# Optimization experiments

Hardware: AMD Instinct MI355X
Metric: run time of the kernel (lower is better)

## Reference

```python
import jax, jax.numpy as jnp
import numpy as np
import math

B, LL, LP, H, C, S, T = 16, 512, 2048, 1024, 8192, 10, 4
PAD_TOKEN_ID = 2000
VAR_TOKEN_BASE = 2001


def _attend(q, k, v):
    # q: [b,q,h], k/v: [b,k,h]
    scores = jnp.einsum('bqh,bkh->bqk', q, k) / math.sqrt(float(q.shape[-1]))
    w = jax.nn.softmax(scores, axis=-1)
    return jnp.einsum('bqk,bkh->bqh', w, v)


def _gru_cell(x, h, Wih, Whh, bih, bhh):
    gi = x @ Wih + bih   # [B,3H], gate order r,z,n (torch GRUCell)
    gh = h @ Whh + bhh
    i_r, i_z, i_n = jnp.split(gi, 3, axis=-1)
    h_r, h_z, h_n = jnp.split(gh, 3, axis=-1)
    r = jax.nn.sigmoid(i_r + h_r)
    z = jax.nn.sigmoid(i_z + h_z)
    n = jnp.tanh(i_n + r * h_n)
    return (1.0 - z) * n + z * h


def setup_inputs() -> dict:
    key = jax.random.key(0)
    ks = jax.random.split(key, 18)
    def lin(k, i, o):
        return jax.random.normal(k, (i, o), jnp.float32) * 0.02
    return {
        'logic_hidden': jax.random.normal(ks[0], (B, LL, H), jnp.float32),
        'prompt_hidden': jax.random.normal(ks[1], (B, LP, H), jnp.float32),
        'codebook_emb': jax.random.normal(ks[2], (C, H), jnp.float32) * 0.02,
        'W_init': lin(ks[3], 2 * H, H),
        'W_pq': lin(ks[4], H, H),
        'W_pk': lin(ks[5], H, H),
        'W_pv': lin(ks[6], H, H),
        'slot_queries': jax.random.normal(ks[7], (S - 1, H), jnp.float32) * 0.02,
        'W_sq': lin(ks[8], H, H),
        'W_op': lin(ks[9], H, H),
        'W_gate': lin(ks[10], H, 1),
        'b_gate': jnp.zeros((1,), jnp.float32),
        'W_stop': lin(ks[11], 2 * H, 1),
        'b_stop': jnp.zeros((1,), jnp.float32),
        'gru_Wih': lin(ks[12], H, 3 * H),
        'gru_Whh': lin(ks[13], H, 3 * H),
        'gru_bih': jnp.zeros((3 * H,), jnp.float32),
        'gru_bhh': jnp.zeros((3 * H,), jnp.float32),
    }


def reference(logic_hidden, prompt_hidden, codebook_emb, W_init, W_pq, W_pk, W_pv,
              slot_queries, W_sq, W_op, W_gate, b_gate, W_stop, b_stop,
              gru_Wih, gru_Whh, gru_bih, gru_bhh):
    batch = logic_hidden.shape[0]
    prompt_summary = prompt_hidden.mean(axis=1)
    logic_summary = logic_hidden.mean(axis=1)
    state = jnp.tanh(jnp.concatenate([prompt_summary, logic_summary], axis=-1) @ W_init)
    pk = prompt_hidden @ W_pk   # [B,LP,H]
    pv = prompt_hidden @ W_pv
    cb_sq = jnp.sum(codebook_emb * codebook_emb, axis=-1)   # [C]
    slot_idx = jnp.arange(S - 1, dtype=jnp.int64)[None, :].repeat(batch, axis=0)

    summaries, stop_logits, stop_probs = [], [], []
    for _ in range(T):
        state_q = (state @ W_pq)[:, None, :]
        state_ctx = _attend(state_q, pk, pv)[:, 0, :]         # [B,H]
        op_pre = state_ctx @ W_op
        # squared euclidean distance to codebook without [B,C,H] diff tensor
        dist = (jnp.sum(op_pre * op_pre, axis=-1, keepdims=True)
                - 2.0 * (op_pre @ codebook_emb.T) + cb_sq[None, :])  # [B,C]
        op_logits = -dist
        op_idx = jnp.argmax(op_logits, axis=-1)               # [B]
        op_embedding = codebook_emb[op_idx]                   # [B,H]
        slot_seed = state_ctx[:, None, :] + slot_queries[None, :, :]   # [B,S-1,H]
        slot_q = slot_seed @ W_sq
        slot_tensors = _attend(slot_q, pk, pv)                # [B,S-1,H]
        slot_use_probs = jax.nn.sigmoid((slot_seed @ W_gate)[..., 0] + b_gate[0])  # [B,S-1]
        slot_mask = slot_use_probs >= 0.5
        # fallback if no slot selected anywhere in the batch (global check, as in torch)
        fb_mask = jax.nn.one_hot(jnp.argmax(slot_use_probs, axis=-1), S - 1, dtype=jnp.bool_)
        slot_mask = jnp.where(jnp.any(slot_mask), slot_mask, fb_mask)
        mf = slot_mask.astype(slot_tensors.dtype)
        slot_summary = jnp.sum(slot_tensors * mf[..., None], axis=1) / \
            jnp.clip(jnp.sum(mf, axis=-1, keepdims=True), 1.0)
        matrix_summary = jnp.tanh(op_embedding + slot_summary)
        stop_logit = (jnp.concatenate([state_ctx, matrix_summary], axis=-1) @ W_stop)[:, 0] + b_stop[0]
        summaries.append(matrix_summary)
        stop_logits.append(stop_logit)
        stop_probs.append(jax.nn.sigmoid(stop_logit))
        state = _gru_cell(matrix_summary, state, gru_Wih, gru_Whh, gru_bih, gru_bhh)

    stop_logits_t = jnp.stack(stop_logits, axis=1)   # [B,T]
    stop_probs_t = jnp.stack(stop_probs, axis=1)
    summary_stack = jnp.stack(summaries, axis=1)     # [B,T,H]
    stop_hits = stop_probs_t >= 0.5
    chain_lengths = jnp.argmax(stop_hits.astype(jnp.int64), axis=1) + 1
    chain_lengths = jnp.where(jnp.sum(stop_hits, axis=1) == 0,
                              jnp.full_like(chain_lengths, T), chain_lengths)
    return summary_stack, stop_logits_t, stop_probs_t, chain_lengths
```

## Files before the change

### kernel.cpp

```cpp
#include <hip/hip_runtime.h>


#define DINL __device__ __forceinline__

DINL float dot4(float4 a, float4 b) {
  return fmaf(a.x, b.x, fmaf(a.y, b.y, fmaf(a.z, b.z, a.w * b.w)));
}
DINL unsigned sortable(float f) {
  unsigned u = __float_as_uint(f);
  return (u & 0x80000000u) ? ~u : (u | 0x80000000u);
}
#define AXPY4(A, W, P) \
  { A.x = fmaf(W, P.x, A.x); A.y = fmaf(W, P.y, A.y); A.z = fmaf(W, P.z, A.z); A.w = fmaf(W, P.w, A.w); }
#define ADD4(A, V) { A.x += V.x; A.y += V.y; A.z += V.z; A.w += V.w; }

static constexpr int F_CBSQ  = 0;
static constexpr int F_STATE = F_CBSQ + 8192;
static constexpr int F_WQK   = F_STATE + 16384;
static constexpr int F_T1    = F_WQK + 1048576;
static constexpr int F_WFUSE = F_T1 + 1048576;
static constexpr int F_SQKCP = F_WFUSE + 2105344;
static constexpr int F_E     = F_SQKCP + 36928;
static constexpr int F_PMP   = F_E + 294912;
static constexpr int F_LMP   = F_PMP + 1048576;
static constexpr int F_MEAN  = F_LMP + 262144;
static constexpr int F_S2P   = F_MEAN + 32768;
static constexpr int F_WQKP  = F_S2P + 131072;
static constexpr int F_T1P   = F_WQKP + 4194304;
static constexpr int F_WFP   = F_T1P + 4194304;
static constexpr int F_QS1   = F_WFP + 8421376;
static constexpr int F_ACCSM = F_QS1 + 131072;
static constexpr int F_LSM   = F_ACCSM + 1048576;
static constexpr int F_CTX   = F_LSM + 1024;
static constexpr int F_FWP   = F_CTX + 16384;
static constexpr int F_OPV   = F_FWP + 526336;
static constexpr int F_OPMAX = F_OPV + 16384;
static constexpr int F_OPIDX = F_OPMAX + 16384;
static constexpr int F_GPRE  = F_OPIDX + 64;
static constexpr int F_GC    = F_GPRE + 64;
static constexpr int F_STOPA = F_GC + 64;
static constexpr int F_QSLB  = F_STOPA + 64;
static constexpr int F_LPS   = F_QSLB + 16384;
static constexpr int F_SSUM  = F_LPS + 4672;
static constexpr int F_MS    = F_SSUM + 16384;
static constexpr int F_GP    = F_MS + 16384;
static constexpr int F_K8P   = F_GP + 786432;
static constexpr int F_ACCP  = F_K8P + 262144;

struct SG {
  const float* Bm;
  const float* Bg;
  const float* a0;
  float* out;
  int M, N, Ncore, NB, kslice, ksh, lda, ldb, ldo, mr;
  float scale;
};

template <int MR>
DINL void sgemm_body(const SG p, int bx, float* As) {
  const int t = threadIdx.x;
  const int ks = bx / p.NB, nb = bx % p.NB;
  const int kslice = p.kslice;
  const int kb = ks * kslice;
  const int tot = p.M * kslice;
  for (int idx = t; idx < tot; idx += 256) {
    const int m = idx >> p.ksh;
    const int kl = idx & (kslice - 1);
    As[(m << p.ksh) + kl] = p.a0[m * p.lda + kb + kl];
  }
  __syncthreads();
  const int nl = t & 63, mg = t >> 6;
  const int n = nb * 64 + nl;
  const bool nok = (n < p.N);
  float acc[MR];
#pragma unroll
  for (int i = 0; i < MR; i++) acc[i] = 0.f;
  const bool useg = nok && (n >= p.Ncore);
  const float* Bc = p.Bm + n;
  for (int k4 = 0; k4 < kslice; k4 += 4) {
    float bv[4];
#pragma unroll
    for (int u = 0; u < 4; u++) {
      bv[u] = 0.f;
      if (nok) bv[u] = useg ? p.Bg[kb + k4 + u] : Bc[(kb + k4 + u) * p.ldb];
    }
#pragma unroll
    for (int i = 0; i < MR; i++) {
      const int m = mg + 4 * i;
      if (MR == 4 || m < p.M) {
        const float4 av = *(const float4*)&As[(m << p.ksh) + k4];
        acc[i] = fmaf(av.x, bv[0], acc[i]);
        acc[i] = fmaf(av.y, bv[1], acc[i]);
        acc[i] = fmaf(av.z, bv[2], acc[i]);
        acc[i] = fmaf(av.w, bv[3], acc[i]);
      }
    }
  }
  if (nok) {
#pragma unroll
    for (int i = 0; i < MR; i++) {
      const int m = mg + 4 * i;
      if (MR == 4 || m < p.M) p.out[(ks * p.M + m) * p.ldo + n] = acc[i] * p.scale;
    }
  }
}

DINL int sw4(int c) { return c ^ (((c >> 5) & 3) << 2); }

DINL void ph_wgT(int bx, float* sm, const float* __restrict__ A1,
                 const float* __restrict__ B, float* __restrict__ C1P,
                 const float* __restrict__ A2, float* __restrict__ C2P) {
  float* As = sm;
  float* Bs = sm + 2112;
  const int which = bx >> 8;
  const int rem = bx & 255;
  const int ks = rem >> 6;
  const int tile = rem & 63;
  const int bi = tile >> 3, bj = tile & 7;
  const float* A = which ? A2 : A1;
  float* CP = (which ? C2P : C1P) + ks * 1048576;
  const int t = threadIdx.x;
  const int sr = t >> 2, q4 = t & 3;
  const int tr = (t >> 4) << 3, tc = (t & 15) << 3;
  const int stc0 = sw4(tc), stc1 = sw4(tc + 4);
  float acc[8][8];
#pragma unroll
  for (int i = 0; i < 8; i++)
#pragma unroll
    for (int j = 0; j < 8; j++) acc[i][j] = 0.f;

  const int k00 = ks * 256;
  for (int k0 = k00; k0 < k00 + 256; k0 += 16) {
    __syncthreads();
#pragma unroll
    for (int h = 0; h < 2; h++) {
      const int r = sr + h * 64;
      const float4 av = *(const float4*)&A[(bi * 128 + r) * 1024 + k0 + q4 * 4];
      const float4 bv = *(const float4*)&B[(bj * 128 + r) * 1024 + k0 + q4 * 4];
      As[(q4 * 4 + 0) * 132 + r] = av.x; As[(q4 * 4 + 1) * 132 + r] = av.y;
      As[(q4 * 4 + 2) * 132 + r] = av.z; As[(q4 * 4 + 3) * 132 + r] = av.w;
      const int swr = sw4(r);
      Bs[(q4 * 4 + 0) * 132 + swr] = bv.x; Bs[(q4 * 4 + 1) * 132 + swr] = bv.y;
      Bs[(q4 * 4 + 2) * 132 + swr] = bv.z; Bs[(q4 * 4 + 3) * 132 + swr] = bv.w;
    }
    __syncthreads();
#pragma unroll
    for (int kk = 0; kk < 16; kk++) {
      const float* ar = &As[kk * 132];
      const float* br = &Bs[kk * 132];
      const float4 a0 = *(const float4*)&ar[tr];
      const float4 a1 = *(const float4*)&ar[tr + 4];
      const float4 b0 = *(const float4*)&br[stc0];
      const float4 b1 = *(const float4*)&br[stc1];
      const float a[8] = {a0.x, a0.y, a0.z, a0.w, a1.x, a1.y, a1.z, a1.w};
      const float b[8] = {b0.x, b0.y, b0.z, b0.w, b1.x, b1.y, b1.z, b1.w};
#pragma unroll
      for (int i = 0; i < 8; i++)
#pragma unroll
        for (int j = 0; j < 8; j++) acc[i][j] = fmaf(a[i], b[j], acc[i][j]);
    }
  }
#pragma unroll
  for (int i = 0; i < 8; i++) {
    const int row = bi * 128 + tr + i;
    *(float4*)&CP[row * 1024 + bj * 128 + tc] =
        make_float4(acc[i][0], acc[i][1], acc[i][2], acc[i][3]);
    *(float4*)&CP[row * 1024 + bj * 128 + tc + 4] =
        make_float4(acc[i][4], acc[i][5], acc[i][6], acc[i][7]);
  }
}

DINL void ph_wgF(int bx, float* sm, const float* __restrict__ Wpv,
                 const float* __restrict__ Wop, const float* __restrict__ T1,
                 float* __restrict__ CfP) {
  float* As = sm;
  float* Bs = sm + 2112;
  const int ks = bx >> 7;
  const int rem = bx & 127;
  const int bi = rem >> 4, bj = rem & 15;
  const float* Bsrc = (bj < 8) ? (Wop + bj * 128) : (T1 + (bj - 8) * 128);
  float* CP = CfP + ks * 2105344;
  const int t = threadIdx.x;
  const int sr = t >> 2, q4 = t & 3;
  const int kkq = t >> 4, c8 = (t & 15) << 3;
  const int tr = (t >> 4) << 3, tc = (t & 15) << 3;
  const int stc0 = sw4(tc), stc1 = sw4(tc + 4);
  float acc[8][8];
#pragma unroll
  for (int i = 0; i < 8; i++)
#pragma unroll
    for (int j = 0; j < 8; j++) acc[i][j] = 0.f;

  const int k00 = ks * 256;
  for (int k0 = k00; k0 < k00 + 256; k0 += 16) {
    __syncthreads();
#pragma unroll
    for (int h = 0; h < 2; h++) {
      const int r = sr + h * 64;
      const float4 av = *(const float4*)&Wpv[(bi * 128 + r) * 1024 + k0 + q4 * 4];
      As[(q4 * 4 + 0) * 132 + r] = av.x; As[(q4 * 4 + 1) * 132 + r] = av.y;
      As[(q4 * 4 + 2) * 132 + r] = av.z; As[(q4 * 4 + 3) * 132 + r] = av.w;
    }
    {
      const float4 v0 = *(const float4*)&Bsrc[(k0 + kkq) * 1024 + c8];
      const float4 v1 = *(const float4*)&Bsrc[(k0 + kkq) * 1024 + c8 + 4];
      *(float4*)&Bs[kkq * 132 + sw4(c8)] = v0;
      *(float4*)&Bs[kkq * 132 + sw4(c8 + 4)] = v1;
    }
    __syncthreads();
#pragma unroll
    for (int kk = 0; kk < 16; kk++) {
      const float* ar = &As[kk * 132];
      const float* br = &Bs[kk * 132];
      const float4 a0 = *(const float4*)&ar[tr];
      const float4 a1 = *(const float4*)&ar[tr + 4];
      const float4 b0 = *(const float4*)&br[stc0];
      const float4 b1 = *(const float4*)&br[stc1];
      const float a[8] = {a0.x, a0.y, a0.z, a0.w, a1.x, a1.y, a1.z, a1.w};
      const float b[8] = {b0.x, b0.y, b0.z, b0.w, b1.x, b1.y, b1.z, b1.w};
#pragma unroll
      for (int i = 0; i < 8; i++)
#pragma unroll
        for (int j = 0; j < 8; j++) acc[i][j] = fmaf(a[i], b[j], acc[i][j]);
    }
  }
#pragma unroll
  for (int i = 0; i < 8; i++) {
    const int row = bi * 128 + tr + i;
    *(float4*)&CP[row * 2056 + bj * 128 + tc] =
        make_float4(acc[i][0], acc[i][1], acc[i][2], acc[i][3]);
    *(float4*)&CP[row * 2056 + bj * 128 + tc + 4] =
        make_float4(acc[i][4], acc[i][5], acc[i][6], acc[i][7]);
  }
}

DINL void ph_meanpsum(int vb, const float* __restrict__ src,
                      float* __restrict__ out, int R) {
  const int s = vb >> 4, b = vb & 15, t = threadIdx.x;
  const float4* base = (const float4*)src + (size_t)(b * R + s * 32) * 256 + t;
  float4 acc = make_float4(0.f, 0.f, 0.f, 0.f);
#pragma unroll 4
  for (int r = 0; r < 32; r++) {
    const float4 v = base[r * 256];
    ADD4(acc, v);
  }
  ((float4*)out)[((s * 16 + b) << 8) + t] = acc;
}

DINL void ph_cbsq(int vb, const float* __restrict__ cbv, float* __restrict__ out) {
  const int c = vb * 4 + (threadIdx.x >> 6);
  const int l = threadIdx.x & 63;
  const float4* cr = (const float4*)(cbv + (c << 10));
  float s = 0.f;
#pragma unroll
  for (int r = 0; r < 4; r++) {
    const float4 v = cr[4 * l + r];
    s += dot4(v, v);
  }
#pragma unroll
  for (int off = 32; off > 0; off >>= 1) s += __shfl_xor(s, off);
  if (l == 0) out[c] = s;
}

DINL void ph_gs(int vb, const float* __restrict__ Wpv, const float* __restrict__ Wgate,
                const float* __restrict__ Wstop, float* __restrict__ Cf) {
  const int t = threadIdx.x;
  const int row = vb * 16 + (t >> 4);
  const int lane = t & 15;
  const float* base = Wpv + row * 1024 + lane * 64;
  const float* gb = Wgate + lane * 64;
  const float* sb = Wstop + lane * 64;
  float g = 0.f, s = 0.f;
#pragma unroll 4
  for (int k = 0; k < 64; k += 4) {
    const float4 av = *(const float4*)&base[k];
    const float4 gv = *(const float4*)&gb[k];
    const float4 sv = *(const float4*)&sb[k];
    g += dot4(av, gv);
    s += dot4(av, sv);
  }
#pragma unroll
  for (int off = 8; off > 0; off >>= 1) {
    g += __shfl_xor(g, off);
    s += __shfl_xor(s, off);
  }
  if (lane == 0) {
    Cf[row * 2056 + 2048] = g;
    Cf[row * 2056 + 2049] = s;
  }
}

DINL void ph_meancat(int vb, const float* __restrict__ pmp,
                     const float* __restrict__ lmp, float* __restrict__ mean) {
  const int gi = vb * 256 + threadIdx.x;
  const int b = gi >> 11, k = gi & 2047;
  float v = 0.f;
  if (k < 1024) {
    for (int s = 0; s < 64; s++) v += pmp[((s * 16 + b) << 10) + k];
    v *= (1.f / 2048.f);
  } else {
    const int kk = k - 1024;
    for (int s = 0; s < 16; s++) v += lmp[((s * 16 + b) << 10) + kk];
    v *= (1.f / 512.f);
  }
  mean[b * 2048 + k] = v;
}

DINL void ph_combT(int vb, const float* __restrict__ C1P, const float* __restrict__ C2P,
                   float* __restrict__ C1, float* __restrict__ C2, float scale) {
  const int half = vb >> 12;
  const int i = ((vb & 4095) << 8) + threadIdx.x;
  const float* src = half ? C2P : C1P;
  float s = 0.f;
#pragma unroll
  for (int ks = 0; ks < 4; ks++) s += src[ks * 1048576 + i];
  (half ? C2 : C1)[i] = s * scale;
}

DINL void ph_combF(int vb, const float* __restrict__ CfP, float* __restrict__ Cf) {
  const int i2 = vb * 256 + threadIdx.x;
  const int r = i2 >> 11, c = i2 & 2047;
  float s = 0.f;
#pragma unroll
  for (int ks = 0; ks < 4; ks++) s += CfP[ks * 2105344 + r * 2056 + c];
  Cf[r * 2056 + c] = s;
}

DINL void ph_s2b(int vb, const float* __restrict__ s2p, float* __restrict__ state) {
  const int gi = vb * 256 + threadIdx.x;
  const int b = gi >> 10, h = gi & 1023;
  float s = 0.f;
  for (int si = 0; si < 8; si++) s += s2p[((si * 16 + b) << 10) + h];
  state[gi] = tanhf(s);
}

DINL void ph_E(int vb, char* qsm, const float* __restrict__ prompt,
               const float* __restrict__ sqkcP, float* __restrict__ E) {
  const int kc = vb & 63, b = vb >> 6;
  const int t = threadIdx.x;
  for (int idx = t; idx < 9216; idx += 256) {
    const int j = idx >> 10, h = idx & 1023;
    float s = 0.f;
    for (int sp = 0; sp < 4; sp++) s += sqkcP[(sp * 9 + j) * 1025 + h];
    const int x = idx << 2;
    *(float*)(qsm + (x ^ (((x >> 7) & 7) << 4))) = s;
  }
  __syncthreads();
  const int w = t >> 6, l = t & 63;
  const int bxl = 64 * l;
  const int key = ((bxl >> 7) & 7) << 4;
  const int o0 = bxl ^ key, o1 = (bxl + 16) ^ key, o2 = (bxl + 32) ^ key, o3 = (bxl + 48) ^ key;
  const int k0 = kc * 32 + w * 8;
  const float* pbase = prompt + ((b * 2048 + k0) << 10) + 16 * l;
  for (int ki = 0; ki < 8; ki++) {
    const float4* pr = (const float4*)(pbase + (ki << 10));
    const float4 p0 = pr[0], p1 = pr[1], p2 = pr[2], p3 = pr[3];
    float sj[9];
#pragma unroll
    for (int j = 0; j < 9; j++) {
      const char* qp = qsm + (j << 12);
      sj[j] = dot4(*(const float4*)(qp + o0), p0) + dot4(*(const float4*)(qp + o1), p1) +
              dot4(*(const float4*)(qp + o2), p2) + dot4(*(const float4*)(qp + o3), p3);
    }
#pragma unroll
    for (int off = 32; off > 0; off >>= 1) {
#pragma unroll
      for (int j = 0; j < 9; j++) sj[j] += __shfl_xor(sj[j], off);
    }
    float wv = sj[0];
#pragma unroll
    for (int j = 1; j < 9; j++)
      if (l == j) wv = sj[j];
    if (l < 9) E[(b * 2048 + k0 + ki) * 9 + l] = __expf(wv);
  }
}

__global__ __launch_bounds__(256) void k_setup1(const float* prompt, const float* logic,
                                                const float* cbv, const float* Wpv,
                                                const float* Wgate, const float* Wstop,
                                                const float* Wpq, const float* Wsq,
                                                const float* Wpk, float* w) {
  __shared__ __align__(16) float sm[4224];
  const int bx = blockIdx.x;
  if (bx < 512) ph_wgT(bx, sm, Wpq, Wpk, w + F_WQKP, Wsq, w + F_T1P);
  else if (bx < 1536) ph_meanpsum(bx - 512, prompt, w + F_PMP, 2048);
  else if (bx < 1792) ph_meanpsum(bx - 1536, logic, w + F_LMP, 512);
  else if (bx < 3840) ph_cbsq(bx - 1792, cbv, w + F_CBSQ);
  else ph_gs(bx - 3840, Wpv, Wgate, Wstop, w + F_WFUSE);
}

__global__ __launch_bounds__(256) void k_setup2(float* w, float scale) {
  const int bx = blockIdx.x;
  if (bx < 8192) ph_combT(bx, w + F_WQKP, w + F_T1P, w + F_WQK, w + F_T1, scale);
  else ph_meancat(bx - 8192, w + F_PMP, w + F_LMP, w + F_MEAN);
}

__global__ __launch_bounds__(256) void k_setup3(SG pInit, SG pSqkc,
                                                const float* Wpv, const float* Wop,
                                                float* w) {
  __shared__ __align__(16) float As[4352];
  const int bx = blockIdx.x;
  if (bx < 512) ph_wgF(bx, As, Wpv, Wop, w + F_T1, w + F_WFP);
  else if (bx < 640) sgemm_body<4>(pInit, bx - 512, As);
  else sgemm_body<7>(pSqkc, bx - 640, As);
}

__global__ __launch_bounds__(256) void k_setup4(const float* prompt, float* w) {
  __shared__ __align__(16) char qsm[36864];
  const int bx = blockIdx.x;
  if (bx < 1024) ph_E(bx, qsm, prompt, w + F_SQKCP, w + F_E);
  else if (bx < 9216) ph_combF(bx - 1024, w + F_WFP, w + F_WFUSE);
  else ph_s2b(bx - 9216, w + F_S2P, w + F_STATE);
}


DINL void ph_qs1(int bx, char* smemc, const float* state, const float* Wqk,
                 float* outP) {
  float* As = (float*)smemc;
  const int t = threadIdx.x;
  const int ks = bx >> 4, nb = bx & 15;
  const int kb = ks * 128;
  for (int idx = t; idx < 2048; idx += 256)
    As[idx] = state[((idx >> 7) << 10) + kb + (idx & 127)];
  __syncthreads();
  const int nl = t & 63, mg = t >> 6;
  const int n = nb * 64 + nl;
  const float* Bc = Wqk + n;
  float acc[4] = {0.f, 0.f, 0.f, 0.f};
  for (int k4 = 0; k4 < 128; k4 += 4) {
    float bv[4];
#pragma unroll
    for (int u = 0; u < 4; u++) bv[u] = Bc[(kb + k4 + u) << 10];
#pragma unroll
    for (int i = 0; i < 4; i++) {
      const float4 av = *(const float4*)&As[((mg + 4 * i) << 7) + k4];
      acc[i] = fmaf(av.x, bv[0], acc[i]);
      acc[i] = fmaf(av.y, bv[1], acc[i]);
      acc[i] = fmaf(av.z, bv[2], acc[i]);
      acc[i] = fmaf(av.w, bv[3], acc[i]);
    }
  }
#pragma unroll
  for (int i = 0; i < 4; i++)
    outP[((ks * 16 + mg + 4 * i) << 10) + n] = acc[i];
}

DINL void ph_flash(int g, int b, char* smemc, const float* prompt,
                   const float* qs1P, float* accsm, float* lsm) {
  float* red = (float*)smemc;
  float* lred = (float*)(smemc + 16384);
  const int t = threadIdx.x;
  const int w = t >> 6, l = t & 63;
  float4 q0 = make_float4(0.f, 0.f, 0.f, 0.f), q1 = q0, q2 = q0, q3 = q0;
#pragma unroll
  for (int s = 0; s < 8; s++) {
    const float4* qp = (const float4*)(qs1P + ((s * 16 + b) << 10) + 16 * l);
    ADD4(q0, qp[0]); ADD4(q1, qp[1]); ADD4(q2, qp[2]); ADD4(q3, qp[3]);
  }
  float4 acc[4];
#pragma unroll
  for (int r = 0; r < 4; r++) acc[r] = make_float4(0.f, 0.f, 0.f, 0.f);
  float lsum = 0.f;
  const int k0 = g * 32 + w * 8;
  const float* pbase = prompt + ((b * 2048 + k0) << 10) + 16 * l;
#pragma unroll 2
  for (int k = 0; k < 8; k++) {
    const float4* pr = (const float4*)(pbase + (k << 10));
    const float4 p0 = pr[0], p1 = pr[1], p2 = pr[2], p3 = pr[3];
    float s = dot4(q0, p0) + dot4(q1, p1) + dot4(q2, p2) + dot4(q3, p3);
#pragma unroll
    for (int off = 32; off > 0; off >>= 1) s += __shfl_xor(s, off);
    const float wgt = __expf(s);
    lsum += wgt;
    AXPY4(acc[0], wgt, p0); AXPY4(acc[1], wgt, p1);
    AXPY4(acc[2], wgt, p2); AXPY4(acc[3], wgt, p3);
  }
  float4* myr = (float4*)(red + w * 1024 + 16 * l);
  myr[0] = acc[0]; myr[1] = acc[1]; myr[2] = acc[2]; myr[3] = acc[3];
  if (l == 0) lred[w] = lsum;
  __syncthreads();
  float4 s0 = *(float4*)(red + t * 4);
  const float4 s1 = *(float4*)(red + 1024 + t * 4);
  const float4 s2 = *(float4*)(red + 2048 + t * 4);
  const float4 s3 = *(float4*)(red + 3072 + t * 4);
  ADD4(s0, s1); ADD4(s0, s2); ADD4(s0, s3);
  *(float4*)&accsm[((b * 64 + g) << 10) + t * 4] = s0;
  if (t == 0) lsm[b * 64 + g] = lred[0] + lred[1] + lred[2] + lred[3];
}

DINL void ph_cst(int bx, char* smemc, const float* accsm, const float* lsm,
                 float* ctx) {
  float4* sred = (float4*)smemc;
  float* rinvp = (float*)(smemc + 4096);
  const int b = bx >> 4, hq = bx & 15;
  const int t = threadIdx.x;
  if (t < 64) {
    float s = lsm[b * 64 + t];
#pragma unroll
    for (int off = 32; off > 0; off >>= 1) s += __shfl_xor(s, off);
    if (t == 0) rinvp[0] = 1.f / s;
  }
  const int h4 = hq * 16 + (t & 15);
  const int gp = t >> 4;
  float4 a = make_float4(0.f, 0.f, 0.f, 0.f);
#pragma unroll
  for (int gi = 0; gi < 4; gi++) {
    const int g = gp * 4 + gi;
    const float4 v = ((const float4*)accsm)[((b * 64 + g) << 8) + h4];
    ADD4(a, v);
  }
  sred[t] = a;
  __syncthreads();
  if (t < 16) {
    float4 s = sred[t];
    for (int p2 = 1; p2 < 16; p2++) {
      const float4 v = sred[p2 * 16 + t];
      ADD4(s, v);
    }
    const float rinv = rinvp[0];
    s.x *= rinv; s.y *= rinv; s.z *= rinv; s.w *= rinv;
    ((float4*)ctx)[(b << 8) + hq * 16 + t] = s;
  }
}

DINL void ph_fw(int bx, char* smemc, const float* ctx, const float* wfuse,
                float* outp) {
  float* As = (float*)smemc;
  const int t = threadIdx.x;
  const int ks = bx / 33, nb = bx % 33;
  const int kb = ks * 64;
  for (int idx = t; idx < 1024; idx += 256)
    As[idx] = ctx[((idx >> 6) << 10) + kb + (idx & 63)];
  __syncthreads();
  const int nl = t & 63, mg = t >> 6;
  const int n = nb * 64 + nl;
  const bool nok = (n < 2050);
  const float* Bc = wfuse + n;
  float acc[4] = {0.f, 0.f, 0.f, 0.f};
  for (int k4 = 0; k4 < 64; k4 += 4) {
    float bv[4];
#pragma unroll
    for (int u = 0; u < 4; u++) bv[u] = nok ? Bc[(kb + k4 + u) * 2056] : 0.f;
#pragma unroll
    for (int i = 0; i < 4; i++) {
      const float4 av = *(const float4*)&As[((mg + 4 * i) << 6) + k4];
      acc[i] = fmaf(av.x, bv[0], acc[i]);
      acc[i] = fmaf(av.y, bv[1], acc[i]);
      acc[i] = fmaf(av.z, bv[2], acc[i]);
      acc[i] = fmaf(av.w, bv[3], acc[i]);
    }
  }
  if (nok) {
#pragma unroll
    for (int i = 0; i < 4; i++) outp[(ks * 16 + mg + 4 * i) * 2056 + n] = acc[i];
  }
}

DINL void ph_combw(int bx, const float* fwP, const float* sqkcP, float* opv,
                   float* qslb, float* gpre, float* gc, float* stopA) {
  const int t = threadIdx.x;
  if (bx < 64) {
    const int i = bx * 256 + t;
    const int b = i >> 10, h = i & 1023;
    float s = 0.f;
    for (int p = 0; p < 16; p++) s += fwP[(p * 16 + b) * 2056 + h];
    opv[i] = s;
  } else if (bx < 128) {
    const int i = (bx - 64) * 256 + t;
    const int b = i >> 10, h = i & 1023;
    float s = 0.f;
    for (int p = 0; p < 16; p++) s += fwP[(p * 16 + b) * 2056 + 1024 + h];
    qslb[i] = s;
  } else {
    if (t < 16) {
      float g = 0.f, sa = 0.f;
      for (int p = 0; p < 16; p++) {
        g += fwP[(p * 16 + t) * 2056 + 2048];
        sa += fwP[(p * 16 + t) * 2056 + 2049];
      }
      gpre[t] = g;
      stopA[t] = sa;
    } else if (t < 25) {
      const int j = t - 16;
      float g = 0.f;
      for (int sp = 0; sp < 4; sp++) g += sqkcP[(sp * 9 + j) * 1025 + 1024];
      gc[j] = g;
    }
  }
}

DINL void ph_slot(int vb, char* smemc, const float* prompt, const float* qslb,
                  const float* E, float* accp, float* lpsum) {
  float* wl = (float*)smemc;
  float* lred = (float*)(smemc + 2560);
  const int kc = vb & 31, b = vb >> 5;
  const int t = threadIdx.x;
  const int w = t >> 6, l = t & 63;
  const float4* qp = (const float4*)(qslb + (b << 10) + 16 * l);
  const float4 q0 = qp[0], q1 = qp[1], q2 = qp[2], q3 = qp[3];
  const int kbase = kc * 64 + w * 16;
  float lacc = 0.f;
  const float* pbase = prompt + ((b * 2048 + kbase) << 10) + 16 * l;
  for (int ki = 0; ki < 16; ki++) {
    const float4* pr = (const float4*)(pbase + (ki << 10));
    const float4 p0 = pr[0], p1 = pr[1], p2 = pr[2], p3 = pr[3];
    float s = dot4(q0, p0) + dot4(q1, p1) + dot4(q2, p2) + dot4(q3, p3);
#pragma unroll
    for (int off = 32; off > 0; off >>= 1) s += __shfl_xor(s, off);
    const float we = __expf(s);
    if (l < 9) {
      const float wv = we * E[(b * 2048 + kbase + ki) * 9 + l];
      wl[(w * 16 + ki) * 10 + l] = wv;
      lacc += wv;
    }
  }
  if (l < 9) lred[w * 9 + l] = lacc;
  __syncthreads();
  if (t < 9)
    lpsum[(b * 32 + kc) * 9 + t] = lred[t] + lred[9 + t] + lred[18 + t] + lred[27 + t];
  const int h4 = (w << 8) + (l << 2);
  float4 acc[9];
#pragma unroll
  for (int j = 0; j < 9; j++) acc[j] = make_float4(0.f, 0.f, 0.f, 0.f);
  const float* pb2 = prompt + ((b * 2048 + kc * 64) << 10) + h4;
#pragma unroll 2
  for (int k = 0; k < 64; k++) {
    const float4 pv = *(const float4*)(pb2 + (k << 10));
    const float* wr = &wl[k * 10];
#pragma unroll
    for (int j = 0; j < 9; j++) AXPY4(acc[j], wr[j], pv);
  }
  float* ob = accp + (((kc * 16 + b) * 9) << 10) + h4;
#pragma unroll
  for (int j = 0; j < 9; j++) *(float4*)(ob + (j << 10)) = acc[j];
}

DINL void ph_cb(int vb, char* smemc, const float* opv, const float* cbv,
                const float* cbsqv, unsigned long long* opmaxp) {
  const int t = threadIdx.x;
  const int w = t >> 6, l = t & 63;
  const int bxl = 64 * l;
  const int key = ((bxl >> 7) & 7) << 4;
  const int o0 = bxl ^ key, o1 = (bxl + 16) ^ key, o2 = (bxl + 32) ^ key, o3 = (bxl + 48) ^ key;
  for (int half = 0; half < 2; half++) {
    __syncthreads();
    for (int idx = t; idx < 8192; idx += 256) {
      const int x = idx << 2;
      *(float*)(smemc + (x ^ (((x >> 7) & 7) << 4))) = opv[half * 8192 + idx];
    }
    __syncthreads();
    unsigned long long bk[8];
#pragma unroll
    for (int m = 0; m < 8; m++) bk[m] = 0ull;
    const int cbase = (vb << 4) + (w << 2);
    for (int ci = 0; ci < 4; ci++) {
      const int c = cbase + ci;
      const float4* cr = (const float4*)(cbv + (c << 10));
      const float4 c0 = cr[4 * l], c1 = cr[4 * l + 1], c2 = cr[4 * l + 2], c3 = cr[4 * l + 3];
      float sm[8];
#pragma unroll
      for (int m = 0; m < 8; m++) {
        const char* qp = smemc + (m << 12);
        const float4 a0 = *(const float4*)(qp + o0);
        const float4 a1 = *(const float4*)(qp + o1);
        const float4 a2 = *(const float4*)(qp + o2);
        const float4 a3 = *(const float4*)(qp + o3);
        sm[m] = dot4(a0, c0) + dot4(a1, c1) + dot4(a2, c2) + dot4(a3, c3);
      }
#pragma unroll
      for (int off = 32; off > 0; off >>= 1) {
#pragma unroll
        for (int m = 0; m < 8; m++) sm[m] += __shfl_xor(sm[m], off);
      }
      const float cq = cbsqv[c];
#pragma unroll
      for (int m = 0; m < 8; m++) {
        const float sc = fmaf(2.f, sm[m], -cq);
        const unsigned long long k2 =
            ((unsigned long long)sortable(sc) << 32) | (unsigned)(8192 - c);
        bk[m] = k2 > bk[m] ? k2 : bk[m];
      }
    }
    unsigned long long* red = (unsigned long long*)(smemc + 32768);
    __syncthreads();
    if (l == 0) {
#pragma unroll
      for (int m = 0; m < 8; m++) red[w * 8 + m] = bk[m];
    }
    __syncthreads();
    if (t < 8) {
      unsigned long long b2 = red[t];
      for (int ww = 1; ww < 4; ww++) {
        const unsigned long long v = red[ww * 8 + t];
        b2 = v > b2 ? v : b2;
      }
      opmaxp[vb * 16 + half * 8 + t] = b2;
    }
  }
}

DINL void ph_k7(int bx, char* smemc, const float* accp, const float* lpsum,
                const float* gpre_g, const float* gc_g, const float* bgate,
                const unsigned long long* opmax, int* opidx, float* ssum) {
  unsigned long long* red = (unsigned long long*)smemc;
  float* rl = (float*)(smemc + 2048);
  float* gpre = (float*)(smemc + 2112);
  float* gcs = (float*)(smemc + 2192);
  int* mask_s = (int*)(smemc + 2240);
  float* cntInvp = (float*)(smemc + 2288);
  const int t = threadIdx.x;
  if (bx == 64) {
    const int b = t & 15, part = t >> 4;
    unsigned long long best = 0ull;
    for (int c = part * 32; c < part * 32 + 32; c++) {
      const unsigned long long v = opmax[c * 16 + b];
      best = v > best ? v : best;
    }
    red[t] = best;
    __syncthreads();
    if (t < 16) {
      unsigned long long m = red[t];
      for (int p2 = 1; p2 < 16; p2++) {
        const unsigned long long v = red[p2 * 16 + t];
        m = v > m ? v : m;
      }
      opidx[t] = 8192 - (int)(unsigned)(m & 0xFFFFFFFFull);
    }
    return;
  }
  const int b = bx >> 2;
  if (t < 9) {
    float s = 0.f;
    for (int c = 0; c < 32; c++) s += lpsum[(b * 32 + c) * 9 + t];
    rl[t] = 1.f / s;
  }
  if (t >= 32 && t < 48) gpre[t - 32] = gpre_g[t - 32];
  if (t >= 48 && t < 57) gcs[t - 48] = gc_g[t - 48];
  __syncthreads();
  if (t == 0) {
    const float bg = bgate[0];
    bool any = false;
    for (int bb = 0; bb < 16; bb++)
      for (int j = 0; j < 9; j++)
        if (gpre[bb] + gcs[j] + bg >= 0.f) any = true;
    int cnt = 0;
    if (any) {
      for (int j = 0; j < 9; j++) {
        const int s = (gpre[b] + gcs[j] + bg >= 0.f) ? 1 : 0;
        mask_s[j] = s;
        cnt += s;
      }
    } else {
      float bv = -3.4e38f;
      int bj = 0;
      for (int j = 0; j < 9; j++) {
        const float v = gpre[b] + gcs[j] + bg;
        if (v > bv) { bv = v; bj = j; }
      }
      for (int j = 0; j < 9; j++) mask_s[j] = (j == bj) ? 1 : 0;
      cnt = 1;
    }
    cntInvp[0] = 1.f / (float)(cnt > 0 ? cnt : 1);
  }
  __syncthreads();
  const int h = ((bx & 3) << 8) + t;
  float v = 0.f;
  for (int j = 0; j < 9; j++) {
    if (mask_s[j]) {
      float s = 0.f;
      for (int c = 0; c < 32; c++) s += accp[(((c * 16 + b) * 9 + j) << 10) + h];
      v = fmaf(s, rl[j], v);
    }
  }
  ssum[(b << 10) + h] = v * cntInvp[0];
}

DINL void ph_k8p(int bx, char* smemc, const float* ssum, const float* Wpv,
                 float* outP) {
  float* As = (float*)smemc;
  const int t = threadIdx.x;
  const int ks = bx >> 4, nb = bx & 15;
  const int kb = ks * 64;
  for (int idx = t; idx < 1024; idx += 256)
    As[idx] = ssum[((idx >> 6) << 10) + kb + (idx & 63)];
  __syncthreads();
  const int nl = t & 63, mg = t >> 6;
  const int n = nb * 64 + nl;
  const float* Bc = Wpv + n;
  float acc[4] = {0.f, 0.f, 0.f, 0.f};
  for (int k4 = 0; k4 < 64; k4 += 4) {
    float bv[4];
#pragma unroll
    for (int u = 0; u < 4; u++) bv[u] = Bc[(kb + k4 + u) << 10];
#pragma unroll
    for (int i = 0; i < 4; i++) {
      const float4 av = *(const float4*)&As[((mg + 4 * i) << 6) + k4];
      acc[i] = fmaf(av.x, bv[0], acc[i]);
      acc[i] = fmaf(av.y, bv[1], acc[i]);
      acc[i] = fmaf(av.z, bv[2], acc[i]);
      acc[i] = fmaf(av.w, bv[3], acc[i]);
    }
  }
#pragma unroll
  for (int i = 0; i < 4; i++)
    outP[((ks * 16 + mg + 4 * i) << 10) + n] = acc[i];
}

DINL void ph_gru(int bx, char* smemc, const float* k8p, const int* opidx,
                 const float* cbv, const float* state, const float* Wih,
                 const float* Whh, float* gpP, float* ms, float* dout, int it) {
  float* As = (float*)smemc;
  const int t = threadIdx.x;
  const int half = (bx >= 384) ? 1 : 0;
  const int b2 = half ? bx - 384 : bx;
  const int ks = b2 / 48, nb = b2 % 48;
  const int kb = ks * 128;
  for (int idx = t; idx < 2048; idx += 256) {
    const int m = idx >> 7, kl = idx & 127;
    float v;
    if (!half) {
      float s = 0.f;
      for (int p = 0; p < 16; p++) s += k8p[((p * 16 + m) << 10) + kb + kl];
      v = tanhf(s + cbv[(opidx[m] << 10) + kb + kl]);
      if (nb == 0) {
        ms[(m << 10) + kb + kl] = v;
        dout[(m << 12) + (it << 10) + kb + kl] = v;
      }
    } else {
      v = state[(m << 10) + kb + kl];
    }
    As[idx] = v;
  }
  __syncthreads();
  const int nl = t & 63, mg = t >> 6;
  const int n = nb * 64 + nl;
  const float* Bc = (half ? Whh : Wih) + n;
  float acc[4] = {0.f, 0.f, 0.f, 0.f};
  for (int k4 = 0; k4 < 128; k4 += 4) {
    float bv[4];
#pragma unroll
    for (int u = 0; u < 4; u++) bv[u] = Bc[(kb + k4 + u) * 3072];
#pragma unroll
    for (int i = 0; i < 4; i++) {
      const float4 av = *(const float4*)&As[((mg + 4 * i) << 7) + k4];
      acc[i] = fmaf(av.x, bv[0], acc[i]);
      acc[i] = fmaf(av.y, bv[1], acc[i]);
      acc[i] = fmaf(av.z, bv[2], acc[i]);
      acc[i] = fmaf(av.w, bv[3], acc[i]);
    }
  }
  float* outp = gpP + half * 3072;
#pragma unroll
  for (int i = 0; i < 4; i++) outp[(ks * 16 + mg + 4 * i) * 6144 + n] = acc[i];
}

DINL void ph_k9b(int bx, const float* gp, const float* bih, const float* bhh,
                 float* state, const float* stopA, const float* ms,
                 const float* Wstop, const float* bstop, float* dout, int it) {
  const int t = threadIdx.x;
  if (bx < 64) {
    const int gi = bx * 256 + t;
    const int b = gi >> 10, h = gi & 1023;
    float ir = 0.f, iz = 0.f, inn = 0.f, hr = 0.f, hz = 0.f, hn = 0.f;
    for (int s = 0; s < 8; s++) {
      const float* g = gp + (s * 16 + b) * 6144;
      ir += g[h]; iz += g[1024 + h]; inn += g[2048 + h];
      hr += g[3072 + h]; hz += g[4096 + h]; hn += g[5120 + h];
    }
    ir += bih[h]; iz += bih[1024 + h]; inn += bih[2048 + h];
    hr += bhh[h]; hz += bhh[1024 + h]; hn += bhh[2048 + h];
    const float r = 1.f / (1.f + __expf(-(ir + hr)));
    const float z = 1.f / (1.f + __expf(-(iz + hz)));
    const float n = tanhf(fmaf(r, hn, inn));
    const float hold = state[gi];
    state[gi] = (1.f - z) * n + z * hold;
  } else {
    const int wid = (bx - 64) * 4 + (t >> 6);
    const int l = t & 63;
    float p = 0.f;
    for (int i = 0; i < 16; i++) {
      const int h = l + (i << 6);
      p = fmaf(ms[(wid << 10) + h], Wstop[1024 + h], p);
    }
#pragma unroll
    for (int off = 32; off > 0; off >>= 1) p += __shfl_xor(p, off);
    if (l == 0) {
      const float lg = p + stopA[wid] + bstop[0];
      dout[65536 + wid * 4 + it] = lg;
      dout[65600 + wid * 4 + it] = 1.f / (1.f + __expf(-lg));
    }
  }
}

__global__ __launch_bounds__(256) void kf_qs1(const float* state, const float* Wqk, float* outP) {
  __shared__ __align__(16) char smem[8192];
  ph_qs1(blockIdx.x, smem, state, Wqk, outP);
}
__global__ __launch_bounds__(256) void kf_flash(const float* prompt, const float* qs1P,
                                                float* accsm, float* lsm) {
  __shared__ __align__(16) char smem[16416];
  ph_flash(blockIdx.x, blockIdx.y, smem, prompt, qs1P, accsm, lsm);
}
__global__ __launch_bounds__(256) void kf_cst(const float* accsm, const float* lsm, float* ctx) {
  __shared__ __align__(16) char smem[4112];
  ph_cst(blockIdx.x, smem, accsm, lsm, ctx);
}
__global__ __launch_bounds__(256) void kf_fw(const float* ctx, const float* wfuse, float* outp) {
  __shared__ __align__(16) char smem[4096];
  ph_fw(blockIdx.x, smem, ctx, wfuse, outp);
}
__global__ __launch_bounds__(256) void kf_combw(const float* fwP, const float* sqkcP,
                                                float* opv, float* qslb, float* gpre,
                                                float* gc, float* stopA) {
  ph_combw(blockIdx.x, fwP, sqkcP, opv, qslb, gpre, gc, stopA);
}
__global__ __launch_bounds__(256) void k_slotcb(const float* prompt, const float* qslb,
                                                const float* E, float* accp, float* lpsum,
                                                const float* opv, const float* cbv,
                                                const float* cbsqv,
                                                unsigned long long* opmaxp) {
  __shared__ __align__(16) char smem[33024];
  const int bx = blockIdx.x;
  if (bx < 512) ph_slot(bx, smem, prompt, qslb, E, accp, lpsum);
  else ph_cb(bx - 512, smem, opv, cbv, cbsqv, opmaxp);
}
__global__ __launch_bounds__(256) void kf_k7(const float* accp, const float* lpsum,
                                             const float* gpre_g, const float* gc_g,
                                             const float* bgate,
                                             const unsigned long long* opmax,
                                             int* opidx, float* ssum) {
  __shared__ __align__(16) char smem[2304];
  ph_k7(blockIdx.x, smem, accp, lpsum, gpre_g, gc_g, bgate, opmax, opidx, ssum);
}
__global__ __launch_bounds__(256) void kf_k8p(const float* ssum, const float* Wpv, float* outP) {
  __shared__ __align__(16) char smem[4096];
  ph_k8p(blockIdx.x, smem, ssum, Wpv, outP);
}
__global__ __launch_bounds__(256) void kf_gru(const float* k8p, const int* opidx,
                                              const float* cbv, const float* state,
                                              const float* Wih, const float* Whh,
                                              float* gpP, float* ms, float* dout, int it) {
  __shared__ __align__(16) char smem[8192];
  ph_gru(blockIdx.x, smem, k8p, opidx, cbv, state, Wih, Whh, gpP, ms, dout, it);
}
__global__ __launch_bounds__(256) void kf_k9b(const float* gp, const float* bih,
                                              const float* bhh, float* state,
                                              const float* stopA, const float* ms,
                                              const float* Wstop, const float* bstop,
                                              float* dout, int it) {
  ph_k9b(blockIdx.x, gp, bih, bhh, state, stopA, ms, Wstop, bstop, dout, it);
}
__global__ void kf_k10(float* __restrict__ dout) {
  const int t = threadIdx.x;
  if (t < 16) {
    int cl = 4;
    for (int it = 0; it < 4; it++) {
      if (dout[65536 + t * 4 + it] >= 0.f) { cl = it + 1; break; }
    }
    dout[65664 + t] = (float)cl;
  }
}

extern "C" void kernel_launch(void* const* d_in, const int* in_sizes, int n_in,
                              void* d_out, int out_size, void* d_ws, size_t ws_size,
                              hipStream_t stream) {
  (void)in_sizes; (void)n_in; (void)out_size; (void)ws_size;
  const float* logic  = (const float*)d_in[0];
  const float* prompt = (const float*)d_in[1];
  const float* cbv    = (const float*)d_in[2];
  const float* W_init = (const float*)d_in[3];
  const float* W_pq   = (const float*)d_in[4];
  const float* W_pk   = (const float*)d_in[5];
  const float* W_pv   = (const float*)d_in[6];
  const float* slotq  = (const float*)d_in[7];
  const float* W_sq   = (const float*)d_in[8];
  const float* W_op   = (const float*)d_in[9];
  const float* W_gate = (const float*)d_in[10];
  const float* b_gate = (const float*)d_in[11];
  const float* W_stop = (const float*)d_in[12];
  const float* b_stop = (const float*)d_in[13];
  const float* Wih    = (const float*)d_in[14];
  const float* Whh    = (const float*)d_in[15];
  const float* bih    = (const float*)d_in[16];
  const float* bhh    = (const float*)d_in[17];
  float* out = (float*)d_out;
  float* w = (float*)d_ws;

  const float inv32 = 1.0f / 32.0f;

  k_setup1<<<3904, 256, 0, stream>>>(prompt, logic, cbv, W_pv, W_gate, W_stop,
                                     W_pq, W_sq, W_pk, w);
  k_setup2<<<8320, 256, 0, stream>>>(w, inv32);
  {
    SG pInit;
    pInit.Bm = W_init; pInit.Bg = nullptr; pInit.a0 = w + F_MEAN;
    pInit.out = w + F_S2P;
    pInit.M = 16; pInit.N = 1024; pInit.Ncore = 1024; pInit.NB = 16;
    pInit.kslice = 256; pInit.ksh = 8; pInit.lda = 2048; pInit.ldb = 1024;
    pInit.ldo = 1024; pInit.mr = 4; pInit.scale = 1.f;
    SG pSqkc;
    pSqkc.Bm = w + F_T1; pSqkc.Bg = W_gate; pSqkc.a0 = slotq;
    pSqkc.out = w + F_SQKCP;
    pSqkc.M = 9; pSqkc.N = 1025; pSqkc.Ncore = 1024; pSqkc.NB = 17;
    pSqkc.kslice = 256; pSqkc.ksh = 8; pSqkc.lda = 1024; pSqkc.ldb = 1024;
    pSqkc.ldo = 1025; pSqkc.mr = 7; pSqkc.scale = 1.f;
    k_setup3<<<708, 256, 0, stream>>>(pInit, pSqkc, W_pv, W_op, w);
  }
  k_setup4<<<9280, 256, 0, stream>>>(prompt, w);

  for (int it = 0; it < 4; ++it) {
    kf_qs1<<<128, 256, 0, stream>>>(w + F_STATE, w + F_WQK, w + F_QS1);
    kf_flash<<<dim3(64, 16), 256, 0, stream>>>(prompt, w + F_QS1,
                                               w + F_ACCSM, w + F_LSM);
    kf_cst<<<256, 256, 0, stream>>>(w + F_ACCSM, w + F_LSM, w + F_CTX);
    kf_fw<<<528, 256, 0, stream>>>(w + F_CTX, w + F_WFUSE, w + F_FWP);
    kf_combw<<<129, 256, 0, stream>>>(w + F_FWP, w + F_SQKCP, w + F_OPV,
                                      w + F_QSLB, w + F_GPRE, w + F_GC, w + F_STOPA);
    k_slotcb<<<1024, 256, 0, stream>>>(prompt, w + F_QSLB, w + F_E,
                                       w + F_ACCP, w + F_LPS, w + F_OPV, cbv,
                                       w + F_CBSQ,
                                       (unsigned long long*)(w + F_OPMAX));
    kf_k7<<<65, 256, 0, stream>>>(w + F_ACCP, w + F_LPS, w + F_GPRE, w + F_GC,
                                  b_gate, (const unsigned long long*)(w + F_OPMAX),
                                  (int*)(w + F_OPIDX), w + F_SSUM);
    kf_k8p<<<256, 256, 0, stream>>>(w + F_SSUM, W_pv, w + F_K8P);
    kf_gru<<<768, 256, 0, stream>>>(w + F_K8P, (const int*)(w + F_OPIDX), cbv,
                                    w + F_STATE, Wih, Whh, w + F_GP, w + F_MS,
                                    out, it);
    kf_k9b<<<68, 256, 0, stream>>>(w + F_GP, bih, bhh, w + F_STATE, w + F_STOPA,
                                   w + F_MS, W_stop, b_stop, out, it);
  }
  kf_k10<<<1, 64, 0, stream>>>(out);
}
```

Measured before the change: 798.6 us.

## Fuse context reduction into fw kernel and double split-K for setup GEMMs

```diff
diff --git a/kernel.cpp b/kernel.cpp
--- a/kernel.cpp
+++ b/kernel.cpp
@@ -26,13 +26,12 @@
 static constexpr int F_MEAN  = F_LMP + 262144;
 static constexpr int F_S2P   = F_MEAN + 32768;
 static constexpr int F_WQKP  = F_S2P + 131072;
-static constexpr int F_T1P   = F_WQKP + 4194304;
-static constexpr int F_WFP   = F_T1P + 4194304;
-static constexpr int F_QS1   = F_WFP + 8421376;
+static constexpr int F_T1P   = F_WQKP + 8388608;
+static constexpr int F_WFP   = F_T1P + 8388608;
+static constexpr int F_QS1   = F_WFP + 16842752;
 static constexpr int F_ACCSM = F_QS1 + 131072;
 static constexpr int F_LSM   = F_ACCSM + 1048576;
-static constexpr int F_CTX   = F_LSM + 1024;
-static constexpr int F_FWP   = F_CTX + 16384;
+static constexpr int F_FWP   = F_LSM + 1024;
 static constexpr int F_OPV   = F_FWP + 526336;
 static constexpr int F_OPMAX = F_OPV + 16384;
 static constexpr int F_OPIDX = F_OPMAX + 16384;
@@ -112,8 +111,8 @@
                  const float* __restrict__ A2, float* __restrict__ C2P) {
   float* As = sm;
   float* Bs = sm + 2112;
-  const int which = bx >> 8;
-  const int rem = bx & 255;
+  const int which = bx >> 9;
+  const int rem = bx & 511;
   const int ks = rem >> 6;
   const int tile = rem & 63;
   const int bi = tile >> 3, bj = tile & 7;
@@ -129,8 +128,8 @@
 #pragma unroll
     for (int j = 0; j < 8; j++) acc[i][j] = 0.f;
 
-  const int k00 = ks * 256;
-  for (int k0 = k00; k0 < k00 + 256; k0 += 16) {
+  const int k00 = ks * 128;
+  for (int k0 = k00; k0 < k00 + 128; k0 += 16) {
     __syncthreads();
 #pragma unroll
     for (int h = 0; h < 2; h++) {
@@ -191,8 +190,8 @@
 #pragma unroll
     for (int j = 0; j < 8; j++) acc[i][j] = 0.f;
 
-  const int k00 = ks * 256;
-  for (int k0 = k00; k0 < k00 + 256; k0 += 16) {
+  const int k00 = ks * 128;
+  for (int k0 = k00; k0 < k00 + 128; k0 += 16) {
     __syncthreads();
 #pragma unroll
     for (int h = 0; h < 2; h++) {
@@ -313,7 +312,7 @@
   const float* src = half ? C2P : C1P;
   float s = 0.f;
 #pragma unroll
-  for (int ks = 0; ks < 4; ks++) s += src[ks * 1048576 + i];
+  for (int ks = 0; ks < 8; ks++) s += src[ks * 1048576 + i];
   (half ? C2 : C1)[i] = s * scale;
 }
 
@@ -322,7 +321,7 @@
   const int r = i2 >> 11, c = i2 & 2047;
   float s = 0.f;
 #pragma unroll
-  for (int ks = 0; ks < 4; ks++) s += CfP[ks * 2105344 + r * 2056 + c];
+  for (int ks = 0; ks < 8; ks++) s += CfP[ks * 2105344 + r * 2056 + c];
   Cf[r * 2056 + c] = s;
 }
 
@@ -382,11 +381,11 @@
                                                 const float* Wpk, float* w) {
   __shared__ __align__(16) float sm[4224];
   const int bx = blockIdx.x;
-  if (bx < 512) ph_wgT(bx, sm, Wpq, Wpk, w + F_WQKP, Wsq, w + F_T1P);
-  else if (bx < 1536) ph_meanpsum(bx - 512, prompt, w + F_PMP, 2048);
-  else if (bx < 1792) ph_meanpsum(bx - 1536, logic, w + F_LMP, 512);
-  else if (bx < 3840) ph_cbsq(bx - 1792, cbv, w + F_CBSQ);
-  else ph_gs(bx - 3840, Wpv, Wgate, Wstop, w + F_WFUSE);
+  if (bx < 1024) ph_wgT(bx, sm, Wpq, Wpk, w + F_WQKP, Wsq, w + F_T1P);
+  else if (bx < 2048) ph_meanpsum(bx - 1024, prompt, w + F_PMP, 2048);
+  else if (bx < 2304) ph_meanpsum(bx - 2048, logic, w + F_LMP, 512);
+  else if (bx < 4352) ph_cbsq(bx - 2304, cbv, w + F_CBSQ);
+  else ph_gs(bx - 4352, Wpv, Wgate, Wstop, w + F_WFUSE);
 }
 
 __global__ __launch_bounds__(256) void k_setup2(float* w, float scale) {
@@ -400,9 +399,9 @@
                                                 float* w) {
   __shared__ __align__(16) float As[4352];
   const int bx = blockIdx.x;
-  if (bx < 512) ph_wgF(bx, As, Wpv, Wop, w + F_T1, w + F_WFP);
-  else if (bx < 640) sgemm_body<4>(pInit, bx - 512, As);
-  else sgemm_body<7>(pSqkc, bx - 640, As);
+  if (bx < 1024) ph_wgF(bx, As, Wpv, Wop, w + F_T1, w + F_WFP);
+  else if (bx < 1152) sgemm_body<4>(pInit, bx - 1024, As);
+  else sgemm_body<7>(pSqkc, bx - 1152, As);
 }
 
 __global__ __launch_bounds__(256) void k_setup4(const float* prompt, float* w) {
@@ -488,49 +487,26 @@
   if (t == 0) lsm[b * 64 + g] = lred[0] + lred[1] + lred[2] + lred[3];
 }
 
-DINL void ph_cst(int bx, char* smemc, const float* accsm, const float* lsm,
-                 float* ctx) {
-  float4* sred = (float4*)smemc;
-  float* rinvp = (float*)(smemc + 4096);
-  const int b = bx >> 4, hq = bx & 15;
-  const int t = threadIdx.x;
-  if (t < 64) {
-    float s = lsm[b * 64 + t];
-#pragma unroll
-    for (int off = 32; off > 0; off >>= 1) s += __shfl_xor(s, off);
-    if (t == 0) rinvp[0] = 1.f / s;
-  }
-  const int h4 = hq * 16 + (t & 15);
-  const int gp = t >> 4;
-  float4 a = make_float4(0.f, 0.f, 0.f, 0.f);
-#pragma unroll
-  for (int gi = 0; gi < 4; gi++) {
-    const int g = gp * 4 + gi;
-    const float4 v = ((const float4*)accsm)[((b * 64 + g) << 8) + h4];
-    ADD4(a, v);
-  }
-  sred[t] = a;
-  __syncthreads();
-  if (t < 16) {
-    float4 s = sred[t];
-    for (int p2 = 1; p2 < 16; p2++) {
-      const float4 v = sred[p2 * 16 + t];
-      ADD4(s, v);
-    }
-    const float rinv = rinvp[0];
-    s.x *= rinv; s.y *= rinv; s.z *= rinv; s.w *= rinv;
-    ((float4*)ctx)[(b << 8) + hq * 16 + t] = s;
-  }
-}
-
-DINL void ph_fw(int bx, char* smemc, const float* ctx, const float* wfuse,
-                float* outp) {
+DINL void ph_fw(int bx, char* smemc, const float* accsm, const float* lsm,
+                const float* wfuse, float* outp) {
   float* As = (float*)smemc;
+  float* rl = (float*)(smemc + 4096);
   const int t = threadIdx.x;
   const int ks = bx / 33, nb = bx % 33;
   const int kb = ks * 64;
-  for (int idx = t; idx < 1024; idx += 256)
-    As[idx] = ctx[((idx >> 6) << 10) + kb + (idx & 63)];
+  if (t < 16) {
+    float s = 0.f;
+    for (int g = 0; g < 64; g++) s += lsm[t * 64 + g];
+    rl[t] = 1.f / s;
+  }
+  __syncthreads();
+  for (int idx = t; idx < 1024; idx += 256) {
+    const int m = idx >> 6;
+    const int h = kb + (idx & 63);
+    float s = 0.f;
+    for (int g = 0; g < 64; g++) s += accsm[((m * 64 + g) << 10) + h];
+    As[idx] = s * rl[m];
+  }
   __syncthreads();
   const int nl = t & 63, mg = t >> 6;
   const int n = nb * 64 + nl;
@@ -901,13 +877,10 @@
   __shared__ __align__(16) char smem[16416];
   ph_flash(blockIdx.x, blockIdx.y, smem, prompt, qs1P, accsm, lsm);
 }
-__global__ __launch_bounds__(256) void kf_cst(const float* accsm, const float* lsm, float* ctx) {
-  __shared__ __align__(16) char smem[4112];
-  ph_cst(blockIdx.x, smem, accsm, lsm, ctx);
-}
-__global__ __launch_bounds__(256) void kf_fw(const float* ctx, const float* wfuse, float* outp) {
-  __shared__ __align__(16) char smem[4096];
-  ph_fw(blockIdx.x, smem, ctx, wfuse, outp);
+__global__ __launch_bounds__(256) void kf_fw(const float* accsm, const float* lsm,
+                                             const float* wfuse, float* outp) {
+  __shared__ __align__(16) char smem[4160];
+  ph_fw(blockIdx.x, smem, accsm, lsm, wfuse, outp);
 }
 __global__ __launch_bounds__(256) void kf_combw(const float* fwP, const float* sqkcP,
                                                 float* opv, float* qslb, float* gpre,
@@ -988,7 +961,7 @@
 
   const float inv32 = 1.0f / 32.0f;
 
-  k_setup1<<<3904, 256, 0, stream>>>(prompt, logic, cbv, W_pv, W_gate, W_stop,
+  k_setup1<<<4416, 256, 0, stream>>>(prompt, logic, cbv, W_pv, W_gate, W_stop,
                                      W_pq, W_sq, W_pk, w);
   k_setup2<<<8320, 256, 0, stream>>>(w, inv32);
   {
@@ -1004,7 +977,7 @@
     pSqkc.M = 9; pSqkc.N = 1025; pSqkc.Ncore = 1024; pSqkc.NB = 17;
     pSqkc.kslice = 256; pSqkc.ksh = 8; pSqkc.lda = 1024; pSqkc.ldb = 1024;
     pSqkc.ldo = 1025; pSqkc.mr = 7; pSqkc.scale = 1.f;
-    k_setup3<<<708, 256, 0, stream>>>(pInit, pSqkc, W_pv, W_op, w);
+    k_setup3<<<1220, 256, 0, stream>>>(pInit, pSqkc, W_pv, W_op, w);
   }
   k_setup4<<<9280, 256, 0, stream>>>(prompt, w);
 
@@ -1012,8 +985,7 @@
     kf_qs1<<<128, 256, 0, stream>>>(w + F_STATE, w + F_WQK, w + F_QS1);
     kf_flash<<<dim3(64, 16), 256, 0, stream>>>(prompt, w + F_QS1,
                                                w + F_ACCSM, w + F_LSM);
-    kf_cst<<<256, 256, 0, stream>>>(w + F_ACCSM, w + F_LSM, w + F_CTX);
-    kf_fw<<<528, 256, 0, stream>>>(w + F_CTX, w + F_WFUSE, w + F_FWP);
+    kf_fw<<<528, 256, 0, stream>>>(w + F_ACCSM, w + F_LSM, w + F_WFUSE, w + F_FWP);
     kf_combw<<<129, 256, 0, stream>>>(w + F_FWP, w + F_SQKCP, w + F_OPV,
                                       w + F_QSLB, w + F_GPRE, w + F_GC, w + F_STOPA);
     k_slotcb<<<1024, 256, 0, stream>>>(prompt, w + F_QSLB, w + F_E,
```

Result: slower. 915.7 us (+14.7%).
